# Performance work log

Hardware: AMD Instinct MI355X
Metric: run time of the kernel (lower is better)

## Reference

```python
import jax, jax.numpy as jnp
import numpy as np

PI = float(np.pi)

def erp_xyz_coords(h, w):
    # matches calculate_erp_coord: pixel grid -> uv -> unit-sphere xyz
    yy, xx = jnp.meshgrid(jnp.linspace(0.0, h - 1.0, h), jnp.linspace(0.0, w - 1.0, w), indexing='ij')
    u = (xx - (w / 2.0 + 0.5)) / w * 2.0 * PI
    v = (yy - (h / 2.0 + 0.5)) / h * PI
    xyz = jnp.stack([jnp.cos(v) * jnp.sin(u), jnp.sin(v), jnp.cos(v) * jnp.cos(u)], axis=-1)
    return xyz.reshape(h * w, 3)  # (HW, 3)


def setup_inputs() -> dict:
    key = jax.random.key(0)
    ks = jax.random.split(key, 16)
    B, C, H, W = 1, 128, 16, 32
    Nkv = 1280
    s = 0.02
    inp = {
        'erp_feature': jax.random.normal(ks[0], (B, C, H, W), jnp.float32),
        'ico_feature': jax.random.normal(ks[1], (B, Nkv, C), jnp.float32),
        'ico_coord': jax.random.normal(ks[2], (B, Nkv, 3), jnp.float32),
        # SA branch params (torch Linear: y = x @ W.T + b, W is (out,in))
        'Wq_sa': jax.random.normal(ks[3], (C, C), jnp.float32) * s,
        'Wkv_sa': jax.random.normal(ks[4], (2 * C, C), jnp.float32) * s,
        'proj_sa_w': jax.random.normal(ks[5], (C, C), jnp.float32) * s,
        'proj_sa_b': jnp.zeros((C,), jnp.float32),
        # DA branch params
        'Wq_da': jax.random.normal(ks[6], (C, C), jnp.float32) * s,
        'Wkv_da': jax.random.normal(ks[7], (2 * C, C), jnp.float32) * s,
        'Wdelta': jax.random.normal(ks[8], (C, 3), jnp.float32) * s,
        'proj_da_w': jax.random.normal(ks[9], (C, C), jnp.float32) * s,
        'proj_da_b': jnp.zeros((C,), jnp.float32),
        # gates
        'gate_sa_w': jax.random.normal(ks[10], (C, 2 * C), jnp.float32) * s,
        'gate_da_w': jax.random.normal(ks[11], (C, 2 * C), jnp.float32) * s,
    }
    return inp


def _forward(erp_feature, ico_feature, ico_coord,
             Wq_sa, Wkv_sa, proj_sa_w, proj_sa_b,
             Wq_da, Wkv_da, Wdelta, proj_da_w, proj_da_b,
             gate_sa_w, gate_da_w):
    B, C, H, W = erp_feature.shape
    Nq = H * W
    q = erp_feature.reshape(B, C, Nq).transpose(0, 2, 1)  # (B, Nq, C)
    qc = erp_xyz_coords(H, W)[None]                        # (1, Nq, 3) broadcasts over B

    # ---- SA branch (iteration = 1) ----
    q_sa = q @ Wq_sa.T                                     # (B, Nq, C)
    kv_sa = (ico_feature @ Wkv_sa.T).reshape(B, -1, 2, C)
    k_sa, v_sa = kv_sa[:, :, 0], kv_sa[:, :, 1]
    attn_sa = jax.nn.softmax(jnp.einsum('bqc,bkc->bqk', q_sa, k_sa) * (C ** -0.5), axis=-1)
    out_sa = jnp.einsum('bqk,bkc->bqc', attn_sa, v_sa)
    # faithful to torch: .transpose(1,2).reshape(B, Nq, C) scrambles layout
    out_sa = out_sa.transpose(0, 2, 1).reshape(B, Nq, C)
    sa = out_sa @ proj_sa_w.T + proj_sa_b

    # ---- DA branch (iteration = 1) ----
    q_da = q @ Wq_da.T
    kv_da = (ico_feature @ Wkv_da.T).reshape(B, -1, 2, C)
    k_da, v_da = kv_da[:, :, 0], kv_da[:, :, 1]
    # feature affinity: sum_c exp(-|q_c - k_c|)   -> (B, Nq, Nkv)
    feat_aff = jnp.exp(-jnp.abs(q_da[:, :, None, :] - k_da[:, None, :, :])).sum(-1)
    # positional term: (exp(-|dq - dk|) @ Wdelta.T).sum(-1) == exp(...) . Wdelta.sum(0)
    pos_exp = jnp.exp(-jnp.abs(qc[:, :, None, :] - ico_coord[:, None, :, :]))  # (B,Nq,Nkv,3)
    pos_aff = jnp.einsum('bqkt,t->bqk', pos_exp, Wdelta.sum(0))
    attn_da = jax.nn.softmax((feat_aff + pos_aff) * (1.0 / C), axis=-1)
    out_da = jnp.einsum('bqk,bkc->bqc', attn_da, v_da)
    da = out_da @ proj_da_w.T + proj_da_b

    # ---- gated fusion ----
    cat = jnp.concatenate([sa, da], axis=-1)               # (B, Nq, 2C)
    sa_factor = jax.nn.sigmoid(cat @ gate_sa_w.T)
    da_factor = jax.nn.sigmoid(cat @ gate_da_w.T)
    fused = sa_factor * sa + da_factor * da                # (B, Nq, C)
    return fused.reshape(B, H, W, C).transpose(0, 3, 1, 2)  # (B, C, H, W)


def reference(erp_feature, ico_feature, ico_coord,
              Wq_sa, Wkv_sa, proj_sa_w, proj_sa_b,
              Wq_da, Wkv_da, Wdelta, proj_da_w, proj_da_b,
              gate_sa_w, gate_da_w):
    return _forward(erp_feature, ico_feature, ico_coord,
                    Wq_sa, Wkv_sa, proj_sa_w, proj_sa_b,
                    Wq_da, Wkv_da, Wdelta, proj_da_w, proj_da_b,
                    gate_sa_w, gate_da_w)
```

## Files before the change

kernel.cpp:

```cpp
#include <hip/hip_runtime.h>
#include <math.h>

#define NQ   512
#define NKV  1280
#define CDIM 128

#define OFF_WDSUM 0
#define OFF_SUMS  16
#define OFF_QSA   1056
#define OFF_QDA   66592
#define OFF_KSAT  132128
#define OFF_VSA   295968
#define OFF_KDAT  459808
#define OFF_VDA   623648
#define OFF_OUT   787488

__global__ __launch_bounds__(256) void prep_kernel(
    const float* __restrict__ erp, const float* __restrict__ ico,
    const float* __restrict__ wq_sa, const float* __restrict__ wq_da,
    const float* __restrict__ wkv_sa, const float* __restrict__ wkv_da,
    const float* __restrict__ wdelta, float* __restrict__ ws)
{
  int bx = blockIdx.x, t = threadIdx.x;
  if (bx < 320) {
    __shared__ float x4[4 * CDIM];
    int k0 = bx * 4;
    for (int i = t; i < 512; i += 256) {
      int ky = i >> 7, j = i & 127;
      x4[j * 4 + ky] = ico[(k0 + ky) * CDIM + j];
    }
    __syncthreads();
    const float4* wsa4 = (const float4*)(wkv_sa + t * CDIM);
    const float4* wda4 = (const float4*)(wkv_da + t * CDIM);
    float as0=0,as1=0,as2=0,as3=0, ad0=0,ad1=0,ad2=0,ad3=0;
    #pragma unroll 4
    for (int j4 = 0; j4 < 32; ++j4) {
      float4 wsv = wsa4[j4];
      float4 wdv = wda4[j4];
      float4 x0 = *(const float4*)&x4[(j4 * 4 + 0) * 4];
      float4 x1 = *(const float4*)&x4[(j4 * 4 + 1) * 4];
      float4 x2 = *(const float4*)&x4[(j4 * 4 + 2) * 4];
      float4 x3 = *(const float4*)&x4[(j4 * 4 + 3) * 4];
      as0 = fmaf(wsv.x, x0.x, as0); as1 = fmaf(wsv.x, x0.y, as1);
      as2 = fmaf(wsv.x, x0.z, as2); as3 = fmaf(wsv.x, x0.w, as3);
      ad0 = fmaf(wdv.x, x0.x, ad0); ad1 = fmaf(wdv.x, x0.y, ad1);
      ad2 = fmaf(wdv.x, x0.z, ad2); ad3 = fmaf(wdv.x, x0.w, ad3);
      as0 = fmaf(wsv.y, x1.x, as0); as1 = fmaf(wsv.y, x1.y, as1);
      as2 = fmaf(wsv.y, x1.z, as2); as3 = fmaf(wsv.y, x1.w, as3);
      ad0 = fmaf(wdv.y, x1.x, ad0); ad1 = fmaf(wdv.y, x1.y, ad1);
      ad2 = fmaf(wdv.y, x1.z, ad2); ad3 = fmaf(wdv.y, x1.w, ad3);
      as0 = fmaf(wsv.z, x2.x, as0); as1 = fmaf(wsv.z, x2.y, as1);
      as2 = fmaf(wsv.z, x2.z, as2); as3 = fmaf(wsv.z, x2.w, as3);
      ad0 = fmaf(wdv.z, x2.x, ad0); ad1 = fmaf(wdv.z, x2.y, ad1);
      ad2 = fmaf(wdv.z, x2.z, ad2); ad3 = fmaf(wdv.z, x2.w, ad3);
      as0 = fmaf(wsv.w, x3.x, as0); as1 = fmaf(wsv.w, x3.y, as1);
      as2 = fmaf(wsv.w, x3.z, as2); as3 = fmaf(wsv.w, x3.w, as3);
      ad0 = fmaf(wdv.w, x3.x, ad0); ad1 = fmaf(wdv.w, x3.y, ad1);
      ad2 = fmaf(wdv.w, x3.z, ad2); ad3 = fmaf(wdv.w, x3.w, ad3);
    }
    if (t < 128) {
      *(float4*)(ws + OFF_KSAT + t * NKV + k0) = make_float4(as0, as1, as2, as3);
      *(float4*)(ws + OFF_KDAT + t * NKV + k0) = make_float4(ad0, ad1, ad2, ad3);
    } else {
      int c = t - 128;
      ws[OFF_VSA + (k0 + 0) * CDIM + c] = as0;
      ws[OFF_VSA + (k0 + 1) * CDIM + c] = as1;
      ws[OFF_VSA + (k0 + 2) * CDIM + c] = as2;
      ws[OFF_VSA + (k0 + 3) * CDIM + c] = as3;
      ws[OFF_VDA + (k0 + 0) * CDIM + c] = ad0;
      ws[OFF_VDA + (k0 + 1) * CDIM + c] = ad1;
      ws[OFF_VDA + (k0 + 2) * CDIM + c] = ad2;
      ws[OFF_VDA + (k0 + 3) * CDIM + c] = ad3;
    }
  } else if (bx < 448) {
    __shared__ float q4[4 * CDIM];
    int n0 = (bx - 320) * 4;
    for (int i = t; i < 512; i += 256)
      q4[i] = erp[(i >> 2) * NQ + n0 + (i & 3)];
    __syncthreads();
    const float* w = (t < 128) ? wq_sa : wq_da;
    int c = t & 127;
    const float4* w4 = (const float4*)(w + c * CDIM);
    float a0 = 0.f, a1 = 0.f, a2 = 0.f, a3 = 0.f;
    #pragma unroll 8
    for (int j4 = 0; j4 < 32; ++j4) {
      float4 wv = w4[j4];
      float4 q0 = *(const float4*)&q4[(j4 * 4 + 0) * 4];
      float4 q1 = *(const float4*)&q4[(j4 * 4 + 1) * 4];
      float4 q2 = *(const float4*)&q4[(j4 * 4 + 2) * 4];
      float4 q3 = *(const float4*)&q4[(j4 * 4 + 3) * 4];
      a0 = fmaf(wv.x, q0.x, a0); a1 = fmaf(wv.x, q0.y, a1);
      a2 = fmaf(wv.x, q0.z, a2); a3 = fmaf(wv.x, q0.w, a3);
      a0 = fmaf(wv.y, q1.x, a0); a1 = fmaf(wv.y, q1.y, a1);
      a2 = fmaf(wv.y, q1.z, a2); a3 = fmaf(wv.y, q1.w, a3);
      a0 = fmaf(wv.z, q2.x, a0); a1 = fmaf(wv.z, q2.y, a1);
      a2 = fmaf(wv.z, q2.z, a2); a3 = fmaf(wv.z, q2.w, a3);
      a0 = fmaf(wv.w, q3.x, a0); a1 = fmaf(wv.w, q3.y, a1);
      a2 = fmaf(wv.w, q3.z, a2); a3 = fmaf(wv.w, q3.w, a3);
    }
    float* o = ws + ((t < 128) ? OFF_QSA : OFF_QDA);
    o[(n0 + 0) * CDIM + c] = a0;
    o[(n0 + 1) * CDIM + c] = a1;
    o[(n0 + 2) * CDIM + c] = a2;
    o[(n0 + 3) * CDIM + c] = a3;
  } else if (bx == 448) {
    *(float4*)(ws + OFF_SUMS + t * 4) = make_float4(0.f, 0.f, 0.f, 0.f);
    if (t < 3) {
      float s = 0.f;
      for (int i = 0; i < 128; ++i) s += wdelta[i * 3 + t];
      ws[OFF_WDSUM + t] = s;
    }
  } else {
    int base = OFF_OUT + (bx - 449) * 1024 + t * 4;
    *(float4*)(ws + base) = make_float4(0.f, 0.f, 0.f, 0.f);
  }
}

__global__ __launch_bounds__(256) void attn_kernel(
    const float* __restrict__ coord, float* __restrict__ ws)
{
  __shared__ __align__(16) float qjf[128][4];
  __shared__ __align__(16) float se[4][256];
  __shared__ float red[4][4];
  __shared__ float qcr[4][3];
  __shared__ float wdl[3];
  int b = blockIdx.x, t = threadIdx.x;
  int br = b & 1;
  int bb = b >> 1;
  int g = bb / 5, z = bb - g * 5;
  int n0 = g * 4, k0 = z * 256;

  const float* qsrc = ws + (br ? OFF_QDA : OFF_QSA);
  {
    int j = t & 127, rh = t >> 7;
    qjf[j][rh]     = qsrc[(n0 + rh)     * CDIM + j];
    qjf[j][rh + 2] = qsrc[(n0 + rh + 2) * CDIM + j];
  }
  if (br) {
    if (t < 4) {
      int n = n0 + t;
      float x = (float)(n & 31), y = (float)(n >> 5);
      float u  = (x - 16.5f) * 0.19634954084936207f;
      float vv = (y -  8.5f) * 0.19634954084936207f;
      float cv = cosf(vv);
      qcr[t][0] = cv * sinf(u);
      qcr[t][1] = sinf(vv);
      qcr[t][2] = cv * cosf(u);
    }
    if (t >= 64 && t < 67) wdl[t - 64] = ws[OFF_WDSUM + (t - 64)];
  }
  __syncthreads();

  int k = k0 + t;
  float acc0 = 0.f, acc1 = 0.f, acc2 = 0.f, acc3 = 0.f;

  if (br) {
    const float* kt = ws + OFF_KDAT + k;
    #pragma unroll 4
    for (int j = 0; j < 128; ++j) {
      float kv = kt[j * NKV];
      float4 q = *(const float4*)qjf[j];
      acc0 += __expf(-fabsf(q.x - kv));
      acc1 += __expf(-fabsf(q.y - kv));
      acc2 += __expf(-fabsf(q.z - kv));
      acc3 += __expf(-fabsf(q.w - kv));
    }
  } else {
    const float* kt = ws + OFF_KSAT + k;
    #pragma unroll 8
    for (int j = 0; j < 128; ++j) {
      float kv = kt[j * NKV];
      float4 q = *(const float4*)qjf[j];
      acc0 = fmaf(q.x, kv, acc0);
      acc1 = fmaf(q.y, kv, acc1);
      acc2 = fmaf(q.z, kv, acc2);
      acc3 = fmaf(q.w, kv, acc3);
    }
  }

  float e0, e1, e2, e3;
  if (br) {
    float c0 = coord[3 * k], c1 = coord[3 * k + 1], c2 = coord[3 * k + 2];
    float w0 = wdl[0], w1 = wdl[1], w2 = wdl[2];
    float p0 = w0 * __expf(-fabsf(qcr[0][0] - c0))
             + w1 * __expf(-fabsf(qcr[0][1] - c1))
             + w2 * __expf(-fabsf(qcr[0][2] - c2));
    float p1 = w0 * __expf(-fabsf(qcr[1][0] - c0))
             + w1 * __expf(-fabsf(qcr[1][1] - c1))
             + w2 * __expf(-fabsf(qcr[1][2] - c2));
    float p2 = w0 * __expf(-fabsf(qcr[2][0] - c0))
             + w1 * __expf(-fabsf(qcr[2][1] - c1))
             + w2 * __expf(-fabsf(qcr[2][2] - c2));
    float p3 = w0 * __expf(-fabsf(qcr[3][0] - c0))
             + w1 * __expf(-fabsf(qcr[3][1] - c1))
             + w2 * __expf(-fabsf(qcr[3][2] - c2));
    const float i128 = 0.0078125f;
    e0 = __expf((acc0 + p0) * i128);
    e1 = __expf((acc1 + p1) * i128);
    e2 = __expf((acc2 + p2) * i128);
    e3 = __expf((acc3 + p3) * i128);
  } else {
    const float scl = 0.088388347648318447f;
    e0 = __expf(acc0 * scl);
    e1 = __expf(acc1 * scl);
    e2 = __expf(acc2 * scl);
    e3 = __expf(acc3 * scl);
  }
  se[0][t] = e0; se[1][t] = e1; se[2][t] = e2; se[3][t] = e3;

  float s0 = e0, s1 = e1, s2 = e2, s3 = e3;
  #pragma unroll
  for (int o = 32; o > 0; o >>= 1) {
    s0 += __shfl_down(s0, o, 64); s1 += __shfl_down(s1, o, 64);
    s2 += __shfl_down(s2, o, 64); s3 += __shfl_down(s3, o, 64);
  }
  if ((t & 63) == 0) {
    int w = t >> 6;
    red[w][0] = s0; red[w][1] = s1; red[w][2] = s2; red[w][3] = s3;
  }
  __syncthreads();
  if (t < 4)
    atomicAdd(ws + OFF_SUMS + br * 512 + n0 + t,
              red[0][t] + red[1][t] + red[2][t] + red[3][t]);

  int c = t & 127, h = t >> 7;
  int kb = h * 128;
  const float* vp = ws + (br ? OFF_VDA : OFF_VSA) + (k0 + kb) * CDIM + c;
  float a0 = 0.f, a1 = 0.f, a2 = 0.f, a3 = 0.f;
  #pragma unroll 2
  for (int ko = 0; ko < 128; ko += 4) {
    float4 p0 = *(const float4*)&se[0][kb + ko];
    float4 p1 = *(const float4*)&se[1][kb + ko];
    float4 p2 = *(const float4*)&se[2][kb + ko];
    float4 p3 = *(const float4*)&se[3][kb + ko];
    float v0 = vp[(ko + 0) * CDIM];
    float v1 = vp[(ko + 1) * CDIM];
    float v2 = vp[(ko + 2) * CDIM];
    float v3 = vp[(ko + 3) * CDIM];
    a0 = fmaf(p0.x, v0, a0); a0 = fmaf(p0.y, v1, a0);
    a0 = fmaf(p0.z, v2, a0); a0 = fmaf(p0.w, v3, a0);
    a1 = fmaf(p1.x, v0, a1); a1 = fmaf(p1.y, v1, a1);
    a1 = fmaf(p1.z, v2, a1); a1 = fmaf(p1.w, v3, a1);
    a2 = fmaf(p2.x, v0, a2); a2 = fmaf(p2.y, v1, a2);
    a2 = fmaf(p2.z, v2, a2); a2 = fmaf(p2.w, v3, a2);
    a3 = fmaf(p3.x, v0, a3); a3 = fmaf(p3.y, v1, a3);
    a3 = fmaf(p3.z, v2, a3); a3 = fmaf(p3.w, v3, a3);
  }
  float* op = ws + OFF_OUT + br * (NQ * CDIM) + c;
  atomicAdd(op + (n0 + 0) * CDIM, a0);
  atomicAdd(op + (n0 + 1) * CDIM, a1);
  atomicAdd(op + (n0 + 2) * CDIM, a2);
  atomicAdd(op + (n0 + 3) * CDIM, a3);
}

__global__ __launch_bounds__(256) void finalize_kernel(
    const float* __restrict__ psa, const float* __restrict__ bsa,
    const float* __restrict__ pda, const float* __restrict__ bda,
    const float* __restrict__ gsa, const float* __restrict__ gda,
    float* __restrict__ out, float* __restrict__ ws)
{
  __shared__ float sain[2][CDIM];
  __shared__ float dain[2][CDIM];
  __shared__ float cat[2][2 * CDIM];
  __shared__ float gl[2][2][CDIM];
  int i0 = blockIdx.x * 2, t = threadIdx.x;
  int h = t >> 7, c = t & 127;
  #pragma unroll
  for (int rr = 0; rr < 2; ++rr) {
    int i = i0 + rr;
    if (h == 0) {
      int row = (i & 3) * 128 + c;
      float s = ws[OFF_SUMS + row];
      sain[rr][c] = ws[OFF_OUT + row * CDIM + (i >> 2)] / s;
    } else {
      float s = ws[OFF_SUMS + 512 + i];
      dain[rr][c] = ws[OFF_OUT + NQ * CDIM + i * CDIM + c] / s;
    }
  }
  __syncthreads();
  {
    const float4* w4 = (const float4*)((h ? pda : psa) + c * CDIM);
    const float* in0 = h ? dain[0] : sain[0];
    const float* in1 = h ? dain[1] : sain[1];
    float a0 = 0, a1 = 0, b0 = 0, b1 = 0;
    #pragma unroll 8
    for (int j4 = 0; j4 < 32; ++j4) {
      float4 wv = w4[j4];
      float4 x0 = *(const float4*)&in0[j4 * 4];
      float4 x1 = *(const float4*)&in1[j4 * 4];
      a0 = fmaf(wv.x, x0.x, a0); a1 = fmaf(wv.y, x0.y, a1);
      a0 = fmaf(wv.z, x0.z, a0); a1 = fmaf(wv.w, x0.w, a1);
      b0 = fmaf(wv.x, x1.x, b0); b1 = fmaf(wv.y, x1.y, b1);
      b0 = fmaf(wv.z, x1.z, b0); b1 = fmaf(wv.w, x1.w, b1);
    }
    float bias = h ? bda[c] : bsa[c];
    cat[0][h * CDIM + c] = bias + a0 + a1;
    cat[1][h * CDIM + c] = bias + b0 + b1;
  }
  __syncthreads();
  {
    const float4* g4 = (const float4*)((h ? gda : gsa) + c * 2 * CDIM);
    float a0 = 0, a1 = 0, b0 = 0, b1 = 0;
    #pragma unroll 8
    for (int j4 = 0; j4 < 64; ++j4) {
      float4 gv = g4[j4];
      float4 c0 = *(const float4*)&cat[0][j4 * 4];
      float4 c1 = *(const float4*)&cat[1][j4 * 4];
      a0 = fmaf(gv.x, c0.x, a0); a1 = fmaf(gv.y, c0.y, a1);
      a0 = fmaf(gv.z, c0.z, a0); a1 = fmaf(gv.w, c0.w, a1);
      b0 = fmaf(gv.x, c1.x, b0); b1 = fmaf(gv.y, c1.y, b1);
      b0 = fmaf(gv.z, c1.z, b0); b1 = fmaf(gv.w, c1.w, b1);
    }
    gl[0][h][c] = 1.0f / (1.0f + __expf(-(a0 + a1)));
    gl[1][h][c] = 1.0f / (1.0f + __expf(-(b0 + b1)));
  }
  __syncthreads();
  {
    int i = i0 + h;
    out[c * NQ + i] = gl[h][0][c] * cat[h][c] + gl[h][1][c] * cat[h][CDIM + c];
  }
}

extern "C" void kernel_launch(void* const* d_in, const int* in_sizes, int n_in,
                              void* d_out, int out_size, void* d_ws, size_t ws_size,
                              hipStream_t stream)
{
  (void)in_sizes; (void)n_in; (void)out_size; (void)ws_size;
  const float* erp       = (const float*)d_in[0];
  const float* ico       = (const float*)d_in[1];
  const float* coord     = (const float*)d_in[2];
  const float* wq_sa     = (const float*)d_in[3];
  const float* wkv_sa    = (const float*)d_in[4];
  const float* proj_sa_w = (const float*)d_in[5];
  const float* proj_sa_b = (const float*)d_in[6];
  const float* wq_da     = (const float*)d_in[7];
  const float* wkv_da    = (const float*)d_in[8];
  const float* wdelta    = (const float*)d_in[9];
  const float* proj_da_w = (const float*)d_in[10];
  const float* proj_da_b = (const float*)d_in[11];
  const float* gate_sa   = (const float*)d_in[12];
  const float* gate_da   = (const float*)d_in[13];
  float* out = (float*)d_out;
  float* ws  = (float*)d_ws;

  hipLaunchKernelGGL(prep_kernel, dim3(577), dim3(256), 0, stream,
                     erp, ico, wq_sa, wq_da, wkv_sa, wkv_da, wdelta, ws);
  hipLaunchKernelGGL(attn_kernel, dim3(1280), dim3(256), 0, stream,
                     coord, ws);
  hipLaunchKernelGGL(finalize_kernel, dim3(256), dim3(256), 0, stream,
                     proj_sa_w, proj_sa_b, proj_da_w, proj_da_b,
                     gate_sa, gate_da, out, ws);
}
```

Before: 147.0 us.

## Retile attention blocks to 8 queries by 128 keys with float4 key loads

Each attention block now covers 8 queries and 128 keys instead of 4 queries and 256 keys. Each thread computes 4 consecutive keys for one query, so K loads become float4 and each V load in the PV loop feeds 8 query accumulators instead of 4. The row-sum reduction becomes a 32-lane shuffle with one atomic per query row, dropping one shared-memory stage. The grid launch count must match the new decomposition, and there are more output atomics per block and more registers per thread.

Result: slower. 157.7 us (+7.3%).

```diff
diff --git a/kernel.cpp b/kernel.cpp
--- a/kernel.cpp
+++ b/kernel.cpp
@@ -119,25 +119,23 @@
 __global__ __launch_bounds__(256) void attn_kernel(
     const float* __restrict__ coord, float* __restrict__ ws)
 {
-  __shared__ __align__(16) float qjf[128][4];
-  __shared__ __align__(16) float se[4][256];
-  __shared__ float red[4][4];
-  __shared__ float qcr[4][3];
+  __shared__ __align__(16) float qjf[128][8];
+  __shared__ __align__(16) float se[8][128];
+  __shared__ float qcr[8][3];
   __shared__ float wdl[3];
   int b = blockIdx.x, t = threadIdx.x;
   int br = b & 1;
   int bb = b >> 1;
-  int g = bb / 5, z = bb - g * 5;
-  int n0 = g * 4, k0 = z * 256;
+  int g = bb / 10, z = bb - g * 10;
+  int n0 = g * 8, k0 = z * 128;
 
   const float* qsrc = ws + (br ? OFF_QDA : OFF_QSA);
-  {
-    int j = t & 127, rh = t >> 7;
-    qjf[j][rh]     = qsrc[(n0 + rh)     * CDIM + j];
-    qjf[j][rh + 2] = qsrc[(n0 + rh + 2) * CDIM + j];
+  for (int i = t; i < 1024; i += 256) {
+    int j = i & 127, r = i >> 7;
+    qjf[j][r] = qsrc[(n0 + r) * CDIM + j];
   }
   if (br) {
-    if (t < 4) {
+    if (t < 8) {
       int n = n0 + t;
       float x = (float)(n & 31), y = (float)(n >> 5);
       float u  = (x - 16.5f) * 0.19634954084936207f;
@@ -151,88 +149,85 @@
   }
   __syncthreads();
 
-  int k = k0 + t;
+  int qd = t & 31, h = t >> 5;
+  int kq = k0 + qd * 4;
   float acc0 = 0.f, acc1 = 0.f, acc2 = 0.f, acc3 = 0.f;
+  float e0, e1, e2, e3;
 
   if (br) {
-    const float* kt = ws + OFF_KDAT + k;
+    const float4* cp = (const float4*)(coord + kq * 3);
+    float4 ca = cp[0], cb = cp[1], cc = cp[2];
+    const float4* kt = (const float4*)(ws + OFF_KDAT + kq);
     #pragma unroll 4
     for (int j = 0; j < 128; ++j) {
-      float kv = kt[j * NKV];
-      float4 q = *(const float4*)qjf[j];
-      acc0 += __expf(-fabsf(q.x - kv));
-      acc1 += __expf(-fabsf(q.y - kv));
-      acc2 += __expf(-fabsf(q.z - kv));
-      acc3 += __expf(-fabsf(q.w - kv));
-    }
-  } else {
-    const float* kt = ws + OFF_KSAT + k;
-    #pragma unroll 8
-    for (int j = 0; j < 128; ++j) {
-      float kv = kt[j * NKV];
-      float4 q = *(const float4*)qjf[j];
-      acc0 = fmaf(q.x, kv, acc0);
-      acc1 = fmaf(q.y, kv, acc1);
-      acc2 = fmaf(q.z, kv, acc2);
-      acc3 = fmaf(q.w, kv, acc3);
-    }
-  }
-
-  float e0, e1, e2, e3;
-  if (br) {
-    float c0 = coord[3 * k], c1 = coord[3 * k + 1], c2 = coord[3 * k + 2];
+      float4 kv = kt[j * (NKV / 4)];
+      float qv = qjf[j][h];
+      acc0 += __expf(-fabsf(qv - kv.x));
+      acc1 += __expf(-fabsf(qv - kv.y));
+      acc2 += __expf(-fabsf(qv - kv.z));
+      acc3 += __expf(-fabsf(qv - kv.w));
+    }
     float w0 = wdl[0], w1 = wdl[1], w2 = wdl[2];
-    float p0 = w0 * __expf(-fabsf(qcr[0][0] - c0))
-             + w1 * __expf(-fabsf(qcr[0][1] - c1))
-             + w2 * __expf(-fabsf(qcr[0][2] - c2));
-    float p1 = w0 * __expf(-fabsf(qcr[1][0] - c0))
-             + w1 * __expf(-fabsf(qcr[1][1] - c1))
-             + w2 * __expf(-fabsf(qcr[1][2] - c2));
-    float p2 = w0 * __expf(-fabsf(qcr[2][0] - c0))
-             + w1 * __expf(-fabsf(qcr[2][1] - c1))
-             + w2 * __expf(-fabsf(qcr[2][2] - c2));
-    float p3 = w0 * __expf(-fabsf(qcr[3][0] - c0))
-             + w1 * __expf(-fabsf(qcr[3][1] - c1))
-             + w2 * __expf(-fabsf(qcr[3][2] - c2));
+    float q0 = qcr[h][0], q1 = qcr[h][1], q2 = qcr[h][2];
+    float p0 = w0 * __expf(-fabsf(q0 - ca.x))
+             + w1 * __expf(-fabsf(q1 - ca.y))
+             + w2 * __expf(-fabsf(q2 - ca.z));
+    float p1 = w0 * __expf(-fabsf(q0 - ca.w))
+             + w1 * __expf(-fabsf(q1 - cb.x))
+             + w2 * __expf(-fabsf(q2 - cb.y));
+    float p2 = w0 * __expf(-fabsf(q0 - cb.z))
+             + w1 * __expf(-fabsf(q1 - cb.w))
+             + w2 * __expf(-fabsf(q2 - cc.x));
+    float p3 = w0 * __expf(-fabsf(q0 - cc.y))
+             + w1 * __expf(-fabsf(q1 - cc.z))
+             + w2 * __expf(-fabsf(q2 - cc.w));
     const float i128 = 0.0078125f;
     e0 = __expf((acc0 + p0) * i128);
     e1 = __expf((acc1 + p1) * i128);
     e2 = __expf((acc2 + p2) * i128);
     e3 = __expf((acc3 + p3) * i128);
   } else {
+    const float4* kt = (const float4*)(ws + OFF_KSAT + kq);
+    #pragma unroll 8
+    for (int j = 0; j < 128; ++j) {
+      float4 kv = kt[j * (NKV / 4)];
+      float qv = qjf[j][h];
+      acc0 = fmaf(qv, kv.x, acc0);
+      acc1 = fmaf(qv, kv.y, acc1);
+      acc2 = fmaf(qv, kv.z, acc2);
+      acc3 = fmaf(qv, kv.w, acc3);
+    }
     const float scl = 0.088388347648318447f;
     e0 = __expf(acc0 * scl);
     e1 = __expf(acc1 * scl);
     e2 = __expf(acc2 * scl);
     e3 = __expf(acc3 * scl);
   }
-  se[0][t] = e0; se[1][t] = e1; se[2][t] = e2; se[3][t] = e3;
-
-  float s0 = e0, s1 = e1, s2 = e2, s3 = e3;
+  *(float4*)&se[h][qd * 4] = make_float4(e0, e1, e2, e3);
+
+  float s = (e0 + e1) + (e2 + e3);
   #pragma unroll
-  for (int o = 32; o > 0; o >>= 1) {
-    s0 += __shfl_down(s0, o, 64); s1 += __shfl_down(s1, o, 64);
-    s2 += __shfl_down(s2, o, 64); s3 += __shfl_down(s3, o, 64);
-  }
-  if ((t & 63) == 0) {
-    int w = t >> 6;
-    red[w][0] = s0; red[w][1] = s1; red[w][2] = s2; red[w][3] = s3;
-  }
-  __syncthreads();
-  if (t < 4)
-    atomicAdd(ws + OFF_SUMS + br * 512 + n0 + t,
-              red[0][t] + red[1][t] + red[2][t] + red[3][t]);
-
-  int c = t & 127, h = t >> 7;
-  int kb = h * 128;
+  for (int o = 16; o > 0; o >>= 1) s += __shfl_down(s, o, 32);
+  if ((t & 31) == 0)
+    atomicAdd(ws + OFF_SUMS + br * 512 + n0 + h, s);
+  __syncthreads();
+
+  int c = t & 127, half = t >> 7;
+  int kb = half * 64;
   const float* vp = ws + (br ? OFF_VDA : OFF_VSA) + (k0 + kb) * CDIM + c;
   float a0 = 0.f, a1 = 0.f, a2 = 0.f, a3 = 0.f;
+  float a4 = 0.f, a5 = 0.f, a6 = 0.f, a7 = 0.f;
   #pragma unroll 2
-  for (int ko = 0; ko < 128; ko += 4) {
-    float4 p0 = *(const float4*)&se[0][kb + ko];
-    float4 p1 = *(const float4*)&se[1][kb + ko];
-    float4 p2 = *(const float4*)&se[2][kb + ko];
-    float4 p3 = *(const float4*)&se[3][kb + ko];
+  for (int ko = 0; ko < 64; ko += 4) {
+    int kk = kb + ko;
+    float4 p0 = *(const float4*)&se[0][kk];
+    float4 p1 = *(const float4*)&se[1][kk];
+    float4 p2 = *(const float4*)&se[2][kk];
+    float4 p3 = *(const float4*)&se[3][kk];
+    float4 p4 = *(const float4*)&se[4][kk];
+    float4 p5 = *(const float4*)&se[5][kk];
+    float4 p6 = *(const float4*)&se[6][kk];
+    float4 p7 = *(const float4*)&se[7][kk];
     float v0 = vp[(ko + 0) * CDIM];
     float v1 = vp[(ko + 1) * CDIM];
     float v2 = vp[(ko + 2) * CDIM];
@@ -245,12 +240,24 @@
     a2 = fmaf(p2.z, v2, a2); a2 = fmaf(p2.w, v3, a2);
     a3 = fmaf(p3.x, v0, a3); a3 = fmaf(p3.y, v1, a3);
     a3 = fmaf(p3.z, v2, a3); a3 = fmaf(p3.w, v3, a3);
+    a4 = fmaf(p4.x, v0, a4); a4 = fmaf(p4.y, v1, a4);
+    a4 = fmaf(p4.z, v2, a4); a4 = fmaf(p4.w, v3, a4);
+    a5 = fmaf(p5.x, v0, a5); a5 = fmaf(p5.y, v1, a5);
+    a5 = fmaf(p5.z, v2, a5); a5 = fmaf(p5.w, v3, a5);
+    a6 = fmaf(p6.x, v0, a6); a6 = fmaf(p6.y, v1, a6);
+    a6 = fmaf(p6.z, v2, a6); a6 = fmaf(p6.w, v3, a6);
+    a7 = fmaf(p7.x, v0, a7); a7 = fmaf(p7.y, v1, a7);
+    a7 = fmaf(p7.z, v2, a7); a7 = fmaf(p7.w, v3, a7);
   }
   float* op = ws + OFF_OUT + br * (NQ * CDIM) + c;
   atomicAdd(op + (n0 + 0) * CDIM, a0);
   atomicAdd(op + (n0 + 1) * CDIM, a1);
   atomicAdd(op + (n0 + 2) * CDIM, a2);
   atomicAdd(op + (n0 + 3) * CDIM, a3);
+  atomicAdd(op + (n0 + 4) * CDIM, a4);
+  atomicAdd(op + (n0 + 5) * CDIM, a5);
+  atomicAdd(op + (n0 + 6) * CDIM, a6);
+  atomicAdd(op + (n0 + 7) * CDIM, a7);
 }
 
 __global__ __launch_bounds__(256) void finalize_kernel(
```

## Split DA attention blocks across half-width key tiles to rebalance work

Applied to the files above, without the earlier changes.

The attention kernel no longer interleaves SA and DA blocks. DA blocks now cover 128 keys each, with the two thread halves handling two query rows apiece, and SA blocks keep 256 keys. The grid grows from 1280 to 1920 blocks, so the expensive exp-based DA affinity work is spread over twice as many blocks and balances against the cheaper SA dot products. Inner loops are also unrolled by hand with batched key loads. The cost is more atomics into the sums and output accumulators, and each DA block reloads the shared query tile.

New measurement: 142.7 us. 2.9% less time.

```diff
diff --git a/kernel.cpp b/kernel.cpp
--- a/kernel.cpp
+++ b/kernel.cpp
@@ -125,17 +125,14 @@
   __shared__ float qcr[4][3];
   __shared__ float wdl[3];
   int b = blockIdx.x, t = threadIdx.x;
-  int br = b & 1;
-  int bb = b >> 1;
-  int g = bb / 5, z = bb - g * 5;
-  int n0 = g * 4, k0 = z * 256;
+  int br = (b < 1280) ? 1 : 0;
+  int n0, k0;
+  if (br) { int g = b / 10;          n0 = g * 4; k0 = (b - g * 10) * 128; }
+  else    { int bb = b - 1280, g = bb / 5; n0 = g * 4; k0 = (bb - g * 5) * 256; }
 
   const float* qsrc = ws + (br ? OFF_QDA : OFF_QSA);
-  {
-    int j = t & 127, rh = t >> 7;
-    qjf[j][rh]     = qsrc[(n0 + rh)     * CDIM + j];
-    qjf[j][rh + 2] = qsrc[(n0 + rh + 2) * CDIM + j];
-  }
+  for (int i = t; i < 512; i += 256)
+    qjf[i >> 2][i & 3] = qsrc[(n0 + (i & 3)) * CDIM + (i >> 2)];
   if (br) {
     if (t < 4) {
       int n = n0 + t;
@@ -151,106 +148,162 @@
   }
   __syncthreads();
 
-  int k = k0 + t;
-  float acc0 = 0.f, acc1 = 0.f, acc2 = 0.f, acc3 = 0.f;
-
   if (br) {
-    const float* kt = ws + OFF_KDAT + k;
-    #pragma unroll 4
-    for (int j = 0; j < 128; ++j) {
-      float kv = kt[j * NKV];
-      float4 q = *(const float4*)qjf[j];
-      acc0 += __expf(-fabsf(q.x - kv));
-      acc1 += __expf(-fabsf(q.y - kv));
-      acc2 += __expf(-fabsf(q.z - kv));
-      acc3 += __expf(-fabsf(q.w - kv));
-    }
-  } else {
-    const float* kt = ws + OFF_KSAT + k;
-    #pragma unroll 8
-    for (int j = 0; j < 128; ++j) {
-      float kv = kt[j * NKV];
-      float4 q = *(const float4*)qjf[j];
-      acc0 = fmaf(q.x, kv, acc0);
-      acc1 = fmaf(q.y, kv, acc1);
-      acc2 = fmaf(q.z, kv, acc2);
-      acc3 = fmaf(q.w, kv, acc3);
-    }
-  }
-
-  float e0, e1, e2, e3;
-  if (br) {
+    int kl = t & 127, rp = t >> 7;
+    int k = k0 + kl, rp2 = rp * 2;
     float c0 = coord[3 * k], c1 = coord[3 * k + 1], c2 = coord[3 * k + 2];
     float w0 = wdl[0], w1 = wdl[1], w2 = wdl[2];
-    float p0 = w0 * __expf(-fabsf(qcr[0][0] - c0))
-             + w1 * __expf(-fabsf(qcr[0][1] - c1))
-             + w2 * __expf(-fabsf(qcr[0][2] - c2));
-    float p1 = w0 * __expf(-fabsf(qcr[1][0] - c0))
-             + w1 * __expf(-fabsf(qcr[1][1] - c1))
-             + w2 * __expf(-fabsf(qcr[1][2] - c2));
-    float p2 = w0 * __expf(-fabsf(qcr[2][0] - c0))
-             + w1 * __expf(-fabsf(qcr[2][1] - c1))
-             + w2 * __expf(-fabsf(qcr[2][2] - c2));
-    float p3 = w0 * __expf(-fabsf(qcr[3][0] - c0))
-             + w1 * __expf(-fabsf(qcr[3][1] - c1))
-             + w2 * __expf(-fabsf(qcr[3][2] - c2));
+    float pA = w0 * __expf(-fabsf(qcr[rp2][0] - c0))
+             + w1 * __expf(-fabsf(qcr[rp2][1] - c1))
+             + w2 * __expf(-fabsf(qcr[rp2][2] - c2));
+    float pB = w0 * __expf(-fabsf(qcr[rp2 + 1][0] - c0))
+             + w1 * __expf(-fabsf(qcr[rp2 + 1][1] - c1))
+             + w2 * __expf(-fabsf(qcr[rp2 + 1][2] - c2));
+    const float* kt = ws + OFF_KDAT + k;
+    float accA = 0.f, accB = 0.f;
+    for (int j8 = 0; j8 < 128; j8 += 8) {
+      float kv0 = kt[(j8 + 0) * NKV];
+      float kv1 = kt[(j8 + 1) * NKV];
+      float kv2 = kt[(j8 + 2) * NKV];
+      float kv3 = kt[(j8 + 3) * NKV];
+      float kv4 = kt[(j8 + 4) * NKV];
+      float kv5 = kt[(j8 + 5) * NKV];
+      float kv6 = kt[(j8 + 6) * NKV];
+      float kv7 = kt[(j8 + 7) * NKV];
+      float2 q0 = *(const float2*)&qjf[j8 + 0][rp2];
+      float2 q1 = *(const float2*)&qjf[j8 + 1][rp2];
+      float2 q2 = *(const float2*)&qjf[j8 + 2][rp2];
+      float2 q3 = *(const float2*)&qjf[j8 + 3][rp2];
+      float2 q4 = *(const float2*)&qjf[j8 + 4][rp2];
+      float2 q5 = *(const float2*)&qjf[j8 + 5][rp2];
+      float2 q6 = *(const float2*)&qjf[j8 + 6][rp2];
+      float2 q7 = *(const float2*)&qjf[j8 + 7][rp2];
+      accA += __expf(-fabsf(q0.x - kv0)); accB += __expf(-fabsf(q0.y - kv0));
+      accA += __expf(-fabsf(q1.x - kv1)); accB += __expf(-fabsf(q1.y - kv1));
+      accA += __expf(-fabsf(q2.x - kv2)); accB += __expf(-fabsf(q2.y - kv2));
+      accA += __expf(-fabsf(q3.x - kv3)); accB += __expf(-fabsf(q3.y - kv3));
+      accA += __expf(-fabsf(q4.x - kv4)); accB += __expf(-fabsf(q4.y - kv4));
+      accA += __expf(-fabsf(q5.x - kv5)); accB += __expf(-fabsf(q5.y - kv5));
+      accA += __expf(-fabsf(q6.x - kv6)); accB += __expf(-fabsf(q6.y - kv6));
+      accA += __expf(-fabsf(q7.x - kv7)); accB += __expf(-fabsf(q7.y - kv7));
+    }
     const float i128 = 0.0078125f;
-    e0 = __expf((acc0 + p0) * i128);
-    e1 = __expf((acc1 + p1) * i128);
-    e2 = __expf((acc2 + p2) * i128);
-    e3 = __expf((acc3 + p3) * i128);
+    float eA = __expf((accA + pA) * i128);
+    float eB = __expf((accB + pB) * i128);
+    se[rp2][kl]     = eA;
+    se[rp2 + 1][kl] = eB;
+    float sA = eA, sB = eB;
+    #pragma unroll
+    for (int o = 32; o > 0; o >>= 1) {
+      sA += __shfl_down(sA, o, 64); sB += __shfl_down(sB, o, 64);
+    }
+    if ((t & 63) == 0) { int w = t >> 6; red[w][0] = sA; red[w][1] = sB; }
+    __syncthreads();
+    if (t < 4) {
+      int base = 2 * (t >> 1);
+      atomicAdd(ws + OFF_SUMS + 512 + n0 + t,
+                red[base][t & 1] + red[base + 1][t & 1]);
+    }
+    int c = t & 127, h = t >> 7;
+    int kb = h * 64;
+    const float* vp = ws + OFF_VDA + (k0 + kb) * CDIM + c;
+    float a0 = 0.f, a1 = 0.f, a2 = 0.f, a3 = 0.f;
+    #pragma unroll 2
+    for (int ko = 0; ko < 64; ko += 4) {
+      int kk = kb + ko;
+      float4 p0 = *(const float4*)&se[0][kk];
+      float4 p1 = *(const float4*)&se[1][kk];
+      float4 p2 = *(const float4*)&se[2][kk];
+      float4 p3 = *(const float4*)&se[3][kk];
+      float v0 = vp[(ko + 0) * CDIM];
+      float v1 = vp[(ko + 1) * CDIM];
+      float v2 = vp[(ko + 2) * CDIM];
+      float v3 = vp[(ko + 3) * CDIM];
+      a0 = fmaf(p0.x, v0, a0); a0 = fmaf(p0.y, v1, a0);
+      a0 = fmaf(p0.z, v2, a0); a0 = fmaf(p0.w, v3, a0);
+      a1 = fmaf(p1.x, v0, a1); a1 = fmaf(p1.y, v1, a1);
+      a1 = fmaf(p1.z, v2, a1); a1 = fmaf(p1.w, v3, a1);
+      a2 = fmaf(p2.x, v0, a2); a2 = fmaf(p2.y, v1, a2);
+      a2 = fmaf(p2.z, v2, a2); a2 = fmaf(p2.w, v3, a2);
+      a3 = fmaf(p3.x, v0, a3); a3 = fmaf(p3.y, v1, a3);
+      a3 = fmaf(p3.z, v2, a3); a3 = fmaf(p3.w, v3, a3);
+    }
+    float* op = ws + OFF_OUT + NQ * CDIM + c;
+    atomicAdd(op + (n0 + 0) * CDIM, a0);
+    atomicAdd(op + (n0 + 1) * CDIM, a1);
+    atomicAdd(op + (n0 + 2) * CDIM, a2);
+    atomicAdd(op + (n0 + 3) * CDIM, a3);
   } else {
+    const float* kt = ws + OFF_KSAT + k0 + t;
+    float acc0 = 0.f, acc1 = 0.f, acc2 = 0.f, acc3 = 0.f;
+    for (int j4 = 0; j4 < 128; j4 += 4) {
+      float kv0 = kt[(j4 + 0) * NKV];
+      float kv1 = kt[(j4 + 1) * NKV];
+      float kv2 = kt[(j4 + 2) * NKV];
+      float kv3 = kt[(j4 + 3) * NKV];
+      float4 q0 = *(const float4*)qjf[j4 + 0];
+      float4 q1 = *(const float4*)qjf[j4 + 1];
+      float4 q2 = *(const float4*)qjf[j4 + 2];
+      float4 q3 = *(const float4*)qjf[j4 + 3];
+      acc0 = fmaf(q0.x, kv0, acc0); acc1 = fmaf(q0.y, kv0, acc1);
+      acc2 = fmaf(q0.z, kv0, acc2); acc3 = fmaf(q0.w, kv0, acc3);
+      acc0 = fmaf(q1.x, kv1, acc0); acc1 = fmaf(q1.y, kv1, acc1);
+      acc2 = fmaf(q1.z, kv1, acc2); acc3 = fmaf(q1.w, kv1, acc3);
+      acc0 = fmaf(q2.x, kv2, acc0); acc1 = fmaf(q2.y, kv2, acc1);
+      acc2 = fmaf(q2.z, kv2, acc2); acc3 = fmaf(q2.w, kv2, acc3);
+      acc0 = fmaf(q3.x, kv3, acc0); acc1 = fmaf(q3.y, kv3, acc1);
+      acc2 = fmaf(q3.z, kv3, acc2); acc3 = fmaf(q3.w, kv3, acc3);
+    }
     const float scl = 0.088388347648318447f;
-    e0 = __expf(acc0 * scl);
-    e1 = __expf(acc1 * scl);
-    e2 = __expf(acc2 * scl);
-    e3 = __expf(acc3 * scl);
-  }
-  se[0][t] = e0; se[1][t] = e1; se[2][t] = e2; se[3][t] = e3;
-
-  float s0 = e0, s1 = e1, s2 = e2, s3 = e3;
-  #pragma unroll
-  for (int o = 32; o > 0; o >>= 1) {
-    s0 += __shfl_down(s0, o, 64); s1 += __shfl_down(s1, o, 64);
-    s2 += __shfl_down(s2, o, 64); s3 += __shfl_down(s3, o, 64);
-  }
-  if ((t & 63) == 0) {
-    int w = t >> 6;
-    red[w][0] = s0; red[w][1] = s1; red[w][2] = s2; red[w][3] = s3;
-  }
-  __syncthreads();
-  if (t < 4)
-    atomicAdd(ws + OFF_SUMS + br * 512 + n0 + t,
-              red[0][t] + red[1][t] + red[2][t] + red[3][t]);
-
-  int c = t & 127, h = t >> 7;
-  int kb = h * 128;
-  const float* vp = ws + (br ? OFF_VDA : OFF_VSA) + (k0 + kb) * CDIM + c;
-  float a0 = 0.f, a1 = 0.f, a2 = 0.f, a3 = 0.f;
-  #pragma unroll 2
-  for (int ko = 0; ko < 128; ko += 4) {
-    float4 p0 = *(const float4*)&se[0][kb + ko];
-    float4 p1 = *(const float4*)&se[1][kb + ko];
-    float4 p2 = *(const float4*)&se[2][kb + ko];
-    float4 p3 = *(const float4*)&se[3][kb + ko];
-    float v0 = vp[(ko + 0) * CDIM];
-    float v1 = vp[(ko + 1) * CDIM];
-    float v2 = vp[(ko + 2) * CDIM];
-    float v3 = vp[(ko + 3) * CDIM];
-    a0 = fmaf(p0.x, v0, a0); a0 = fmaf(p0.y, v1, a0);
-    a0 = fmaf(p0.z, v2, a0); a0 = fmaf(p0.w, v3, a0);
-    a1 = fmaf(p1.x, v0, a1); a1 = fmaf(p1.y, v1, a1);
-    a1 = fmaf(p1.z, v2, a1); a1 = fmaf(p1.w, v3, a1);
-    a2 = fmaf(p2.x, v0, a2); a2 = fmaf(p2.y, v1, a2);
-    a2 = fmaf(p2.z, v2, a2); a2 = fmaf(p2.w, v3, a2);
-    a3 = fmaf(p3.x, v0, a3); a3 = fmaf(p3.y, v1, a3);
-    a3 = fmaf(p3.z, v2, a3); a3 = fmaf(p3.w, v3, a3);
-  }
-  float* op = ws + OFF_OUT + br * (NQ * CDIM) + c;
-  atomicAdd(op + (n0 + 0) * CDIM, a0);
-  atomicAdd(op + (n0 + 1) * CDIM, a1);
-  atomicAdd(op + (n0 + 2) * CDIM, a2);
-  atomicAdd(op + (n0 + 3) * CDIM, a3);
+    float e0 = __expf(acc0 * scl);
+    float e1 = __expf(acc1 * scl);
+    float e2 = __expf(acc2 * scl);
+    float e3 = __expf(acc3 * scl);
+    se[0][t] = e0; se[1][t] = e1; se[2][t] = e2; se[3][t] = e3;
+    float s0 = e0, s1 = e1, s2 = e2, s3 = e3;
+    #pragma unroll
+    for (int o = 32; o > 0; o >>= 1) {
+      s0 += __shfl_down(s0, o, 64); s1 += __shfl_down(s1, o, 64);
+      s2 += __shfl_down(s2, o, 64); s3 += __shfl_down(s3, o, 64);
+    }
+    if ((t & 63) == 0) {
+      int w = t >> 6;
+      red[w][0] = s0; red[w][1] = s1; red[w][2] = s2; red[w][3] = s3;
+    }
+    __syncthreads();
+    if (t < 4)
+      atomicAdd(ws + OFF_SUMS + n0 + t,
+                red[0][t] + red[1][t] + red[2][t] + red[3][t]);
+    int c = t & 127, h = t >> 7;
+    int kb = h * 128;
+    const float* vp = ws + OFF_VSA + (k0 + kb) * CDIM + c;
+    float a0 = 0.f, a1 = 0.f, a2 = 0.f, a3 = 0.f;
+    #pragma unroll 2
+    for (int ko = 0; ko < 128; ko += 4) {
+      int kk = kb + ko;
+      float4 p0 = *(const float4*)&se[0][kk];
+      float4 p1 = *(const float4*)&se[1][kk];
+      float4 p2 = *(const float4*)&se[2][kk];
+      float4 p3 = *(const float4*)&se[3][kk];
+      float v0 = vp[(ko + 0) * CDIM];
+      float v1 = vp[(ko + 1) * CDIM];
+      float v2 = vp[(ko + 2) * CDIM];
+      float v3 = vp[(ko + 3) * CDIM];
+      a0 = fmaf(p0.x, v0, a0); a0 = fmaf(p0.y, v1, a0);
+      a0 = fmaf(p0.z, v2, a0); a0 = fmaf(p0.w, v3, a0);
+      a1 = fmaf(p1.x, v0, a1); a1 = fmaf(p1.y, v1, a1);
+      a1 = fmaf(p1.z, v2, a1); a1 = fmaf(p1.w, v3, a1);
+      a2 = fmaf(p2.x, v0, a2); a2 = fmaf(p2.y, v1, a2);
+      a2 = fmaf(p2.z, v2, a2); a2 = fmaf(p2.w, v3, a2);
+      a3 = fmaf(p3.x, v0, a3); a3 = fmaf(p3.y, v1, a3);
+      a3 = fmaf(p3.z, v2, a3); a3 = fmaf(p3.w, v3, a3);
+    }
+    float* op = ws + OFF_OUT + c;
+    atomicAdd(op + (n0 + 0) * CDIM, a0);
+    atomicAdd(op + (n0 + 1) * CDIM, a1);
+    atomicAdd(op + (n0 + 2) * CDIM, a2);
+    atomicAdd(op + (n0 + 3) * CDIM, a3);
+  }
 }
 
 __global__ __launch_bounds__(256) void finalize_kernel(
@@ -345,7 +398,7 @@
 
   hipLaunchKernelGGL(prep_kernel, dim3(577), dim3(256), 0, stream,
                      erp, ico, wq_sa, wq_da, wkv_sa, wkv_da, wdelta, ws);
-  hipLaunchKernelGGL(attn_kernel, dim3(1280), dim3(256), 0, stream,
+  hipLaunchKernelGGL(attn_kernel, dim3(1920), dim3(256), 0, stream,
                      coord, ws);
   hipLaunchKernelGGL(finalize_kernel, dim3(256), dim3(256), 0, stream,
                      proj_sa_w, proj_sa_b, proj_da_w, proj_da_b,
```
